# Performance work log

Measured on AMD Instinct MI355X. Metric: run time of the kernel, lower is better.

The kernel has to match this reference:

```python
import jax, jax.numpy as jnp
import numpy as np

B, N, M, F_DIM, H, D = 4, 2048, 2048, 512, 8, 64  # M == num_time
MID = H * D
EPS = 1e-5


def _layernorm(x, w, b):
    mu = jnp.mean(x, axis=-1, keepdims=True)
    var = jnp.var(x, axis=-1, keepdims=True)
    return (x - mu) * jax.lax.rsqrt(var + EPS) * w + b


def setup_inputs() -> dict:
    key = jax.random.key(0)
    ks = jax.random.split(key, 12)
    s = 0.02
    return {
        "x": jax.random.normal(ks[0], (B, N, F_DIM), jnp.float32),
        "context": jax.random.normal(ks[1], (B, M, F_DIM), jnp.float32),
        "pos_emb": jax.random.normal(ks[2], (M, F_DIM), jnp.float32) * s,  # nn.Embedding(num_time, features)
        "ln_w": jnp.ones((F_DIM,), jnp.float32),
        "ln_b": jnp.zeros((F_DIM,), jnp.float32),
        "lnc_w": jnp.ones((F_DIM,), jnp.float32),
        "lnc_b": jnp.zeros((F_DIM,), jnp.float32),
        "Wq": jax.random.normal(ks[3], (F_DIM, MID), jnp.float32) * s,
        "Wk": jax.random.normal(ks[4], (F_DIM, MID), jnp.float32) * s,
        "Wv": jax.random.normal(ks[5], (F_DIM, MID), jnp.float32) * s,
        "Wout": jax.random.normal(ks[6], (MID, F_DIM), jnp.float32) * s,
        "bout": jnp.zeros((F_DIM,), jnp.float32),
    }


def reference(x, context, pos_emb, ln_w, ln_b, lnc_w, lnc_b, Wq, Wk, Wv, Wout, bout):
    scale = D ** (-0.5)
    keys = jnp.broadcast_to(pos_emb[None], (x.shape[0], M, F_DIM))  # [B, T, F]
    xn = _layernorm(x, ln_w, ln_b)
    kn = _layernorm(keys, ln_w, ln_b)          # same norm as x (self.norm)
    cn = _layernorm(context, lnc_w, lnc_b)
    q = (xn @ Wq).reshape(x.shape[0], N, H, D).transpose(0, 2, 1, 3)  # b h n d
    k = (kn @ Wk).reshape(x.shape[0], M, H, D).transpose(0, 2, 1, 3)  # b h m d
    v = (cn @ Wv).reshape(x.shape[0], M, H, D).transpose(0, 2, 1, 3)  # b h m d
    sim = jnp.einsum('bhnd,bhmd->bhnm', q, k) * scale
    attn = jax.nn.softmax(sim, axis=-1)
    out = jnp.einsum('bhnm,bhmd->bhnd', attn, v)
    out = out.transpose(0, 2, 1, 3).reshape(x.shape[0], N, MID)  # b n (h d)
    return out @ Wout + bout
```

## Files before the change

kernel.cpp:

```cpp
#include <hip/hip_runtime.h>
#include <stdint.h>

#define B_ 4
#define N_ 2048
#define M_ 2048
#define F_ 512
#define H_ 8
#define D_ 64

typedef __bf16 bf16x8 __attribute__((ext_vector_type(8)));
typedef float f32x4 __attribute__((ext_vector_type(4)));
typedef float f32x16 __attribute__((ext_vector_type(16)));

typedef const __attribute__((address_space(1))) uint32_t* gas_ptr;
typedef __attribute__((address_space(3))) uint32_t* las_ptr;

__device__ inline ushort f32_bf16(float f) {
    union { float f; uint32_t u; } v; v.f = f;
    uint32_t r = v.u + 0x7FFFu + ((v.u >> 16) & 1u);
    return (ushort)(r >> 16);
}

__global__ __launch_bounds__(128) void ln_kernel(
    const float* __restrict__ x, const float* __restrict__ ctx, const float* __restrict__ pos,
    const float* __restrict__ lnw, const float* __restrict__ lnb,
    const float* __restrict__ lncw, const float* __restrict__ lncb,
    ushort* __restrict__ xn, ushort* __restrict__ kn, ushort* __restrict__ cn)
{
    int r = blockIdx.x;
    const float* src; ushort* dst; const float* w; const float* bp;
    if (r < B_ * N_) {
        src = x + (size_t)r * F_; dst = xn + (size_t)r * F_; w = lnw; bp = lnb;
    } else if (r < B_ * N_ + M_) {
        int rr = r - B_ * N_;
        src = pos + (size_t)rr * F_; dst = kn + (size_t)rr * F_; w = lnw; bp = lnb;
    } else {
        int rr = r - (B_ * N_ + M_);
        src = ctx + (size_t)rr * F_; dst = cn + (size_t)rr * F_; w = lncw; bp = lncb;
    }
    int tid = threadIdx.x;
    int wave = tid >> 6, lane = tid & 63;
    float4 v = reinterpret_cast<const float4*>(src)[tid];
    float s = v.x + v.y + v.z + v.w;
    float sq = v.x * v.x + v.y * v.y + v.z * v.z + v.w * v.w;
    #pragma unroll
    for (int mask = 1; mask < 64; mask <<= 1) {
        s += __shfl_xor(s, mask, 64);
        sq += __shfl_xor(sq, mask, 64);
    }
    __shared__ float red[4];
    if (lane == 0) { red[wave * 2] = s; red[wave * 2 + 1] = sq; }
    __syncthreads();
    float S = red[0] + red[2], SQ = red[1] + red[3];
    float mean = S * (1.0f / F_);
    float var = SQ * (1.0f / F_) - mean * mean;
    float rstd = rsqrtf(var + 1e-5f);
    float4 wv = reinterpret_cast<const float4*>(w)[tid];
    float4 bv = reinterpret_cast<const float4*>(bp)[tid];
    ushort4 o;
    o.x = f32_bf16((v.x - mean) * rstd * wv.x + bv.x);
    o.y = f32_bf16((v.y - mean) * rstd * wv.y + bv.y);
    o.z = f32_bf16((v.z - mean) * rstd * wv.z + bv.z);
    o.w = f32_bf16((v.w - mean) * rstd * wv.w + bv.w);
    reinterpret_cast<ushort4*>(dst)[tid] = o;
}

__global__ __launch_bounds__(256) void wtrans_kernel(
    const float* __restrict__ Wq, const float* __restrict__ Wk,
    const float* __restrict__ Wv, const float* __restrict__ Wo,
    ushort* __restrict__ WqT, ushort* __restrict__ WkT,
    ushort* __restrict__ WvT, ushort* __restrict__ WoT)
{
    const float* W; ushort* WT;
    switch (blockIdx.z) {
        case 0: W = Wq; WT = WqT; break;
        case 1: W = Wk; WT = WkT; break;
        case 2: W = Wv; WT = WvT; break;
        default: W = Wo; WT = WoT; break;
    }
    __shared__ float tile[32][33];
    int tx = threadIdx.x, ty = threadIdx.y;
    int n0 = blockIdx.x * 32, k0 = blockIdx.y * 32;
    #pragma unroll
    for (int j = 0; j < 4; ++j)
        tile[ty + j * 8][tx] = W[(size_t)(k0 + ty + j * 8) * F_ + n0 + tx];
    __syncthreads();
    #pragma unroll
    for (int j = 0; j < 4; ++j)
        WT[(size_t)(n0 + ty + j * 8) * F_ + k0 + tx] = f32_bf16(tile[tx][ty + j * 8]);
}

__device__ __forceinline__ void gemm_body(
    const ushort* __restrict__ A, const ushort* __restrict__ BT,
    const float* __restrict__ bias, void* __restrict__ Cout,
    int mode, int bx, int by)
{
    __shared__ ushort As[128][64];
    __shared__ ushort Bs[128][64];
    int tid = threadIdx.x;
    int row0 = by * 128, col0 = bx * 128;
    int wv = tid >> 6, lane = tid & 63;
    int wm = wv >> 1, wn = wv & 1;
    f32x4 acc[4][4] = {};

    const int lrow8 = lane >> 3;
    const int chs = ((lane & 7) ^ (lrow8 & 7)) * 8;
    const ushort* agp = A + (size_t)(row0 + wv * 32 + lrow8) * F_ + chs;
    const ushort* bgp = BT + (size_t)(col0 + wv * 32 + lrow8) * F_ + chs;

    for (int k0 = 0; k0 < F_; k0 += 64) {
        #pragma unroll
        for (int j = 0; j < 4; ++j) {
            __builtin_amdgcn_global_load_lds(
                (gas_ptr)(const void*)(agp + k0 + j * 8 * F_),
                (las_ptr)(void*)&As[wv * 32 + j * 8][0], 16, 0, 0);
            __builtin_amdgcn_global_load_lds(
                (gas_ptr)(const void*)(bgp + k0 + j * 8 * F_),
                (las_ptr)(void*)&Bs[wv * 32 + j * 8][0], 16, 0, 0);
        }
        __syncthreads();
        #pragma unroll
        for (int kt = 0; kt < 2; ++kt) {
            int lrow = lane & 15;
            int ch = ((kt * 4 + (lane >> 4)) ^ (lane & 7)) * 8;
            bf16x8 af[4], bfr[4];
            #pragma unroll
            for (int mt = 0; mt < 4; ++mt)
                af[mt] = *reinterpret_cast<const bf16x8*>(&As[wm * 64 + mt * 16 + lrow][ch]);
            #pragma unroll
            for (int nt = 0; nt < 4; ++nt)
                bfr[nt] = *reinterpret_cast<const bf16x8*>(&Bs[wn * 64 + nt * 16 + lrow][ch]);
            #pragma unroll
            for (int mt = 0; mt < 4; ++mt)
                #pragma unroll
                for (int nt = 0; nt < 4; ++nt)
                    acc[mt][nt] = __builtin_amdgcn_mfma_f32_16x16x32_bf16(
                        af[mt], bfr[nt], acc[mt][nt], 0, 0, 0);
        }
        __syncthreads();
    }

    int lr4 = (lane >> 4) * 4, lc = lane & 15;
    #pragma unroll
    for (int mt = 0; mt < 4; ++mt) {
        #pragma unroll
        for (int nt = 0; nt < 4; ++nt) {
            int ccol = col0 + wn * 64 + nt * 16 + lc;
            float bv = (mode == 1) ? bias[ccol] : 0.0f;
            #pragma unroll
            for (int j = 0; j < 4; ++j) {
                int crow = row0 + wm * 64 + mt * 16 + lr4 + j;
                float val = acc[mt][nt][j] + bv;
                if (mode == 1) {
                    reinterpret_cast<float*>(Cout)[(size_t)crow * F_ + ccol] = val;
                } else if (mode == 0) {
                    reinterpret_cast<ushort*>(Cout)[(size_t)crow * F_ + ccol] = f32_bf16(val);
                } else if (mode == 2) {
                    int h = ccol >> 6, t = crow >> 7, s = (crow >> 6) & 1;
                    int ab = (crow >> 5) & 1, l31 = crow & 31;
                    int ds = (ccol >> 4) & 3, g2 = (ccol >> 3) & 1, e = ccol & 7;
                    size_t addr = (((size_t)(h * 16 + t) * 16 + s * 8 + ds * 2 + ab) * 64
                                   + g2 * 32 + l31) * 8 + e;
                    reinterpret_cast<ushort*>(Cout)[addr] = f32_bf16(val);
                } else {
                    int b2 = crow >> 11, m = crow & 2047;
                    int h = ccol >> 6, d = ccol & 63;
                    int bh = b2 * 8 + h, hh = d >> 5, l31 = d & 31;
                    int t = m >> 7, s = (m >> 6) & 1, s_ = (m >> 4) & 3;
                    int g2 = (m >> 3) & 1, i = m & 7;
                    size_t addr = (((size_t)(bh * 16 + t) * 16 + hh * 8 + s * 4 + s_) * 64
                                   + g2 * 32 + l31) * 8 + i;
                    reinterpret_cast<ushort*>(Cout)[addr] = f32_bf16(val);
                }
            }
        }
    }
}

__global__ __launch_bounds__(256) void qkv_gemm_kernel(
    const ushort* __restrict__ xn, const ushort* __restrict__ kn,
    const ushort* __restrict__ cn,
    const ushort* __restrict__ WqT, const ushort* __restrict__ WkT,
    const ushort* __restrict__ WvT,
    ushort* __restrict__ qb, ushort* __restrict__ kF, ushort* __restrict__ vF)
{
    int bid = blockIdx.x;
    if (bid < 256) {
        gemm_body(xn, WqT, nullptr, (void*)qb, 0, bid & 3, bid >> 2);
    } else if (bid < 320) {
        int t = bid - 256;
        gemm_body(kn, WkT, nullptr, (void*)kF, 2, t & 3, t >> 2);
    } else {
        int t = bid - 320;
        gemm_body(cn, WvT, nullptr, (void*)vF, 3, t & 3, t >> 2);
    }
}

__global__ __launch_bounds__(256) void out_gemm_kernel(
    const ushort* __restrict__ A, const ushort* __restrict__ WoT,
    const float* __restrict__ bias, float* __restrict__ out)
{
    gemm_body(A, WoT, bias, (void*)out, 1, blockIdx.x & 3, blockIdx.x >> 2);
}

#define MAKE_PA(dst, p, ss) do {                                               \
    uint32_t w0_, w1_, w2_, w3_;                                               \
    asm("v_cvt_pk_bf16_f32 %0, %1, %2" : "=v"(w0_) : "v"(p[8*(ss)+0]), "v"(p[8*(ss)+1])); \
    asm("v_cvt_pk_bf16_f32 %0, %1, %2" : "=v"(w1_) : "v"(p[8*(ss)+2]), "v"(p[8*(ss)+3])); \
    asm("v_cvt_pk_bf16_f32 %0, %1, %2" : "=v"(w2_) : "v"(p[8*(ss)+4]), "v"(p[8*(ss)+5])); \
    asm("v_cvt_pk_bf16_f32 %0, %1, %2" : "=v"(w3_) : "v"(p[8*(ss)+6]), "v"(p[8*(ss)+7])); \
    asm("v_permlane32_swap_b32 %0, %1" : "+v"(w0_), "+v"(w2_));                \
    asm("v_permlane32_swap_b32 %0, %1" : "+v"(w1_), "+v"(w3_));                \
    union { uint32_t w[4]; bf16x8 v; } u_;                                     \
    u_.w[0] = w0_; u_.w[1] = w1_; u_.w[2] = w2_; u_.w[3] = w3_;                \
    dst = u_.v;                                                                \
} while (0)

#define KLOAD(DST, u) do {                                                     \
    const ushort* _p = kfb_ + (size_t)(u) * 4096 + lane * 8;                   \
    _Pragma("unroll")                                                          \
    for (int f_ = 0; f_ < 8; ++f_)                                             \
        DST[f_] = *reinterpret_cast<const bf16x8*>(_p + f_ * 512);             \
} while (0)

#define VLOAD(DST, u) do {                                                     \
    const ushort* _p = vfb_ + (size_t)((u) >> 1) * 8192 +                      \
                       ((u) & 1) * 4 * 512 + lane * 8;                         \
    _Pragma("unroll")                                                          \
    for (int hh_ = 0; hh_ < 2; ++hh_)                                          \
        _Pragma("unroll")                                                      \
        for (int s2_ = 0; s2_ < 4; ++s2_)                                      \
            DST[hh_ * 4 + s2_] = *reinterpret_cast<const bf16x8*>(             \
                _p + (hh_ * 8 + s2_) * 512);                                   \
} while (0)

#define COMPUTE_ONE(QF, OACC, LR) do {                                         \
    f32x16 sA, sB;                                                             \
    _Pragma("unroll")                                                          \
    for (int j = 0; j < 16; ++j) { sA[j] = 0.0f; sB[j] = 0.0f; }               \
    __builtin_amdgcn_s_setprio(1);                                             \
    _Pragma("unroll")                                                          \
    for (int ds_ = 0; ds_ < 4; ++ds_) {                                        \
        sA = __builtin_amdgcn_mfma_f32_32x32x16_bf16(kR[ds_ * 2], QF[ds_], sA, 0, 0, 0); \
        sB = __builtin_amdgcn_mfma_f32_32x32x16_bf16(kR[ds_ * 2 + 1], QF[ds_], sB, 0, 0, 0); \
    }                                                                          \
    __builtin_amdgcn_s_setprio(0);                                             \
    float p0f[16], p1f[16];                                                    \
    _Pragma("unroll")                                                          \
    for (int j = 0; j < 16; ++j)                                               \
        p0f[j] = __builtin_amdgcn_exp2f(sA[j] * c1);                           \
    _Pragma("unroll")                                                          \
    for (int j = 0; j < 16; ++j)                                               \
        p1f[j] = __builtin_amdgcn_exp2f(sB[j] * c1);                           \
    float r0 = 0.0f, r1 = 0.0f, r2 = 0.0f, r3 = 0.0f;                          \
    _Pragma("unroll")                                                          \
    for (int j = 0; j < 16; j += 4) {                                          \
        r0 += p0f[j];     r1 += p0f[j + 1];                                    \
        r2 += p0f[j + 2]; r3 += p0f[j + 3];                                    \
    }                                                                          \
    _Pragma("unroll")                                                          \
    for (int j = 0; j < 16; j += 4) {                                          \
        r0 += p1f[j];     r1 += p1f[j + 1];                                    \
        r2 += p1f[j + 2]; r3 += p1f[j + 3];                                    \
    }                                                                          \
    LR += (r0 + r1) + (r2 + r3);                                               \
    bf16x8 pa[4];                                                              \
    MAKE_PA(pa[0], p0f, 0);                                                    \
    MAKE_PA(pa[1], p0f, 1);                                                    \
    MAKE_PA(pa[2], p1f, 0);                                                    \
    MAKE_PA(pa[3], p1f, 1);                                                    \
    __builtin_amdgcn_s_setprio(1);                                             \
    _Pragma("unroll")                                                          \
    for (int hh = 0; hh < 2; ++hh)                                             \
        _Pragma("unroll")                                                      \
        for (int s_ = 0; s_ < 4; ++s_)                                         \
            OACC[hh] = __builtin_amdgcn_mfma_f32_32x32x16_bf16(                \
                pa[s_], vR[hh * 4 + s_], OACC[hh], 0, 0, 0);                   \
    __builtin_amdgcn_s_setprio(0);                                             \
} while (0)

__global__ __launch_bounds__(512, 1) void attn_kernel(
    const ushort* __restrict__ q,
    const ushort* __restrict__ kF,
    const ushort* __restrict__ vF,
    ushort* __restrict__ o)
{
    const int wave = threadIdx.x >> 6, lane = threadIdx.x & 63;
    const int l31 = lane & 31, g = lane >> 5;
    const int qpair = wave & 3, half = wave >> 2;
    const int bid = blockIdx.x;
    const int qx = bid >> 5, bh = bid & 31;
    const int b = bh >> 3, h = bh & 7;
    const int q0 = qx * 256 + qpair * 64;

    __shared__ float ols[4][64][64];
    __shared__ float lls[4][2][64];

    bf16x8 qfA[4], qfB[4];
    const ushort* qrowA = q + (size_t)(b * N_ + q0 + l31) * F_ + h * 64 + g * 8;
    const ushort* qrowB = qrowA + 32 * F_;
    #pragma unroll
    for (int ds = 0; ds < 4; ++ds) {
        qfA[ds] = *reinterpret_cast<const bf16x8*>(qrowA + ds * 16);
        qfB[ds] = *reinterpret_cast<const bf16x8*>(qrowB + ds * 16);
    }

    float l0 = 0.0f, l1 = 0.0f;
    f32x16 oaccA[2], oaccB[2];
    #pragma unroll
    for (int hh = 0; hh < 2; ++hh)
        #pragma unroll
        for (int j = 0; j < 16; ++j) { oaccA[hh][j] = 0.0f; oaccB[hh][j] = 0.0f; }

    const ushort* kfb_ = kF + (size_t)h * 16 * 16 * 512;
    const ushort* vfb_ = vF + (size_t)bh * 16 * 16 * 512;
    const float c1 = 0.18033688f;

    bf16x8 kR[8], vR[8];
    const int ubase = half * 16;

    #pragma unroll 1
    for (int uu = 0; uu < 16; ++uu) {
        int u = ubase + uu;
        KLOAD(kR, u);
        VLOAD(vR, u);
        COMPUTE_ONE(qfA, oaccA, l0);
        COMPUTE_ONE(qfB, oaccB, l1);
    }

    l0 += __shfl_xor(l0, 32, 64);
    l1 += __shfl_xor(l1, 32, 64);

    if (half) {
        #pragma unroll
        for (int hh = 0; hh < 2; ++hh)
            #pragma unroll
            for (int j = 0; j < 16; ++j) {
                ols[qpair][hh * 16 + j][lane] = oaccA[hh][j];
                ols[qpair][32 + hh * 16 + j][lane] = oaccB[hh][j];
            }
        lls[qpair][0][lane] = l0;
        lls[qpair][1][lane] = l1;
    }
    __syncthreads();
    if (!half) {
        #pragma unroll
        for (int hh = 0; hh < 2; ++hh)
            #pragma unroll
            for (int j = 0; j < 16; ++j) {
                oaccA[hh][j] += ols[qpair][hh * 16 + j][lane];
                oaccB[hh][j] += ols[qpair][32 + hh * 16 + j][lane];
            }
        l0 += lls[qpair][0][lane];
        l1 += lls[qpair][1][lane];
        float li0 = 1.0f / l0, li1 = 1.0f / l1;
        float rli0[16], rli1[16];
        #pragma unroll
        for (int j = 0; j < 16; ++j) {
            int idx = 8 * (j >> 2) + 4 * g + (j & 3);
            rli0[j] = __shfl(li0, idx, 64);
            rli1[j] = __shfl(li1, idx, 64);
        }
        #pragma unroll
        for (int hh = 0; hh < 2; ++hh)
            #pragma unroll
            for (int j = 0; j < 16; ++j) {
                int qr = (j & 3) + 8 * (j >> 2) + 4 * g;
                o[(size_t)(b * N_ + q0 + qr) * F_ + h * 64 + hh * 32 + l31] =
                    f32_bf16(oaccA[hh][j] * rli0[j]);
                o[(size_t)(b * N_ + q0 + 32 + qr) * F_ + h * 64 + hh * 32 + l31] =
                    f32_bf16(oaccB[hh][j] * rli1[j]);
            }
    }
}

extern "C" void kernel_launch(void* const* d_in, const int* in_sizes, int n_in,
                              void* d_out, int out_size, void* d_ws, size_t ws_size,
                              hipStream_t stream) {
    const float* x    = (const float*)d_in[0];
    const float* ctx  = (const float*)d_in[1];
    const float* pos  = (const float*)d_in[2];
    const float* lnw  = (const float*)d_in[3];
    const float* lnb  = (const float*)d_in[4];
    const float* lncw = (const float*)d_in[5];
    const float* lncb = (const float*)d_in[6];
    const float* Wq   = (const float*)d_in[7];
    const float* Wk   = (const float*)d_in[8];
    const float* Wv   = (const float*)d_in[9];
    const float* Wo   = (const float*)d_in[10];
    const float* bout = (const float*)d_in[11];
    float* out = (float*)d_out;

    char* ws = (char*)d_ws;
    ushort* xn  = (ushort*)(ws + 0);
    ushort* cn  = (ushort*)(ws + 8388608);
    ushort* kn  = (ushort*)(ws + 16777216);
    ushort* WqT = (ushort*)(ws + 18874368);
    ushort* WkT = (ushort*)(ws + 19398656);
    ushort* WvT = (ushort*)(ws + 19922944);
    ushort* WoT = (ushort*)(ws + 20447232);
    ushort* qb  = (ushort*)(ws + 20971520);
    ushort* kFb = (ushort*)(ws + 29360128);
    ushort* vFb = (ushort*)(ws + 39845888);
    ushort* ao  = (ushort*)(ws + 48234496);

    hipLaunchKernelGGL(ln_kernel, dim3(B_ * N_ + M_ + B_ * M_), dim3(128), 0, stream,
                       x, ctx, pos, lnw, lnb, lncw, lncb, xn, kn, cn);
    hipLaunchKernelGGL(wtrans_kernel, dim3(16, 16, 4), dim3(32, 8), 0, stream,
                       Wq, Wk, Wv, Wo, WqT, WkT, WvT, WoT);
    hipLaunchKernelGGL(qkv_gemm_kernel, dim3(576), dim3(256), 0, stream,
                       xn, kn, cn, WqT, WkT, WvT, qb, kFb, vFb);
    hipLaunchKernelGGL(attn_kernel, dim3(256), dim3(512), 0, stream,
                       qb, kFb, vFb, ao);
    hipLaunchKernelGGL(out_gemm_kernel, dim3(256), dim3(256), 0, stream,
                       ao, WoT, bout, out);
}
```

Before: 101.5 us.

## Merge layernorm and weight transpose kernels; split attention compute into halves

Combines the layernorm and weight-transpose launches into a single prep kernel whose grid covers both jobs, removing one kernel launch and its inter-kernel gap. The attention inner loop is also split so each call handles one 32-key half (one S tile, exp, P pack, PV), interleaving the two query groups. This lowers live register pressure for the S/P arrays and may give the scheduler more overlap between MFMA and exp work, at the cost of more, smaller dependency chains.

```diff
diff --git a/kernel.cpp b/kernel.cpp
--- a/kernel.cpp
+++ b/kernel.cpp
@@ -21,73 +21,76 @@
     return (ushort)(r >> 16);
 }
 
-__global__ __launch_bounds__(128) void ln_kernel(
+__global__ __launch_bounds__(128) void prep_kernel(
     const float* __restrict__ x, const float* __restrict__ ctx, const float* __restrict__ pos,
     const float* __restrict__ lnw, const float* __restrict__ lnb,
     const float* __restrict__ lncw, const float* __restrict__ lncb,
-    ushort* __restrict__ xn, ushort* __restrict__ kn, ushort* __restrict__ cn)
-{
-    int r = blockIdx.x;
-    const float* src; ushort* dst; const float* w; const float* bp;
-    if (r < B_ * N_) {
-        src = x + (size_t)r * F_; dst = xn + (size_t)r * F_; w = lnw; bp = lnb;
-    } else if (r < B_ * N_ + M_) {
-        int rr = r - B_ * N_;
-        src = pos + (size_t)rr * F_; dst = kn + (size_t)rr * F_; w = lnw; bp = lnb;
-    } else {
-        int rr = r - (B_ * N_ + M_);
-        src = ctx + (size_t)rr * F_; dst = cn + (size_t)rr * F_; w = lncw; bp = lncb;
-    }
-    int tid = threadIdx.x;
-    int wave = tid >> 6, lane = tid & 63;
-    float4 v = reinterpret_cast<const float4*>(src)[tid];
-    float s = v.x + v.y + v.z + v.w;
-    float sq = v.x * v.x + v.y * v.y + v.z * v.z + v.w * v.w;
-    #pragma unroll
-    for (int mask = 1; mask < 64; mask <<= 1) {
-        s += __shfl_xor(s, mask, 64);
-        sq += __shfl_xor(sq, mask, 64);
-    }
-    __shared__ float red[4];
-    if (lane == 0) { red[wave * 2] = s; red[wave * 2 + 1] = sq; }
-    __syncthreads();
-    float S = red[0] + red[2], SQ = red[1] + red[3];
-    float mean = S * (1.0f / F_);
-    float var = SQ * (1.0f / F_) - mean * mean;
-    float rstd = rsqrtf(var + 1e-5f);
-    float4 wv = reinterpret_cast<const float4*>(w)[tid];
-    float4 bv = reinterpret_cast<const float4*>(bp)[tid];
-    ushort4 o;
-    o.x = f32_bf16((v.x - mean) * rstd * wv.x + bv.x);
-    o.y = f32_bf16((v.y - mean) * rstd * wv.y + bv.y);
-    o.z = f32_bf16((v.z - mean) * rstd * wv.z + bv.z);
-    o.w = f32_bf16((v.w - mean) * rstd * wv.w + bv.w);
-    reinterpret_cast<ushort4*>(dst)[tid] = o;
-}
-
-__global__ __launch_bounds__(256) void wtrans_kernel(
     const float* __restrict__ Wq, const float* __restrict__ Wk,
     const float* __restrict__ Wv, const float* __restrict__ Wo,
+    ushort* __restrict__ xn, ushort* __restrict__ kn, ushort* __restrict__ cn,
     ushort* __restrict__ WqT, ushort* __restrict__ WkT,
     ushort* __restrict__ WvT, ushort* __restrict__ WoT)
 {
+    __shared__ float red[4];
+    __shared__ float tile[32][33];
+    int r = blockIdx.x;
+    int tid = threadIdx.x;
+
+    if (r < B_ * N_ + M_ + B_ * M_) {
+        const float* src; ushort* dst; const float* w; const float* bp;
+        if (r < B_ * N_) {
+            src = x + (size_t)r * F_; dst = xn + (size_t)r * F_; w = lnw; bp = lnb;
+        } else if (r < B_ * N_ + M_) {
+            int rr = r - B_ * N_;
+            src = pos + (size_t)rr * F_; dst = kn + (size_t)rr * F_; w = lnw; bp = lnb;
+        } else {
+            int rr = r - (B_ * N_ + M_);
+            src = ctx + (size_t)rr * F_; dst = cn + (size_t)rr * F_; w = lncw; bp = lncb;
+        }
+        int wave = tid >> 6, lane = tid & 63;
+        float4 v = reinterpret_cast<const float4*>(src)[tid];
+        float s = v.x + v.y + v.z + v.w;
+        float sq = v.x * v.x + v.y * v.y + v.z * v.z + v.w * v.w;
+        #pragma unroll
+        for (int mask = 1; mask < 64; mask <<= 1) {
+            s += __shfl_xor(s, mask, 64);
+            sq += __shfl_xor(sq, mask, 64);
+        }
+        if (lane == 0) { red[wave * 2] = s; red[wave * 2 + 1] = sq; }
+        __syncthreads();
+        float S = red[0] + red[2], SQ = red[1] + red[3];
+        float mean = S * (1.0f / F_);
+        float var = SQ * (1.0f / F_) - mean * mean;
+        float rstd = rsqrtf(var + 1e-5f);
+        float4 wv = reinterpret_cast<const float4*>(w)[tid];
+        float4 bv = reinterpret_cast<const float4*>(bp)[tid];
+        ushort4 o;
+        o.x = f32_bf16((v.x - mean) * rstd * wv.x + bv.x);
+        o.y = f32_bf16((v.y - mean) * rstd * wv.y + bv.y);
+        o.z = f32_bf16((v.z - mean) * rstd * wv.z + bv.z);
+        o.w = f32_bf16((v.w - mean) * rstd * wv.w + bv.w);
+        reinterpret_cast<ushort4*>(dst)[tid] = o;
+        return;
+    }
+
+    int wblk = r - (B_ * N_ + M_ + B_ * M_);
     const float* W; ushort* WT;
-    switch (blockIdx.z) {
+    switch (wblk >> 8) {
         case 0: W = Wq; WT = WqT; break;
         case 1: W = Wk; WT = WkT; break;
         case 2: W = Wv; WT = WvT; break;
         default: W = Wo; WT = WoT; break;
     }
-    __shared__ float tile[32][33];
-    int tx = threadIdx.x, ty = threadIdx.y;
-    int n0 = blockIdx.x * 32, k0 = blockIdx.y * 32;
+    int ti = wblk & 255;
+    int n0 = (ti & 15) * 32, k0 = (ti >> 4) * 32;
+    int tx = tid & 31, ty = tid >> 5;
     #pragma unroll
-    for (int j = 0; j < 4; ++j)
-        tile[ty + j * 8][tx] = W[(size_t)(k0 + ty + j * 8) * F_ + n0 + tx];
+    for (int j = 0; j < 8; ++j)
+        tile[ty + j * 4][tx] = W[(size_t)(k0 + ty + j * 4) * F_ + n0 + tx];
     __syncthreads();
     #pragma unroll
-    for (int j = 0; j < 4; ++j)
-        WT[(size_t)(n0 + ty + j * 8) * F_ + k0 + tx] = f32_bf16(tile[tx][ty + j * 8]);
+    for (int j = 0; j < 8; ++j)
+        WT[(size_t)(n0 + ty + j * 4) * F_ + k0 + tx] = f32_bf16(tile[tx][ty + j * 4]);
 }
 
 __device__ __forceinline__ void gemm_body(
@@ -234,48 +237,37 @@
                 _p + (hh_ * 8 + s2_) * 512);                                   \
 } while (0)
 
-#define COMPUTE_ONE(QF, OACC, LR) do {                                         \
-    f32x16 sA, sB;                                                             \
-    _Pragma("unroll")                                                          \
-    for (int j = 0; j < 16; ++j) { sA[j] = 0.0f; sB[j] = 0.0f; }               \
+#define COMPUTE_HALF(QF, OACC, LR, AB) do {                                    \
+    f32x16 sS;                                                                 \
+    _Pragma("unroll")                                                          \
+    for (int j = 0; j < 16; ++j) sS[j] = 0.0f;                                 \
     __builtin_amdgcn_s_setprio(1);                                             \
     _Pragma("unroll")                                                          \
-    for (int ds_ = 0; ds_ < 4; ++ds_) {                                        \
-        sA = __builtin_amdgcn_mfma_f32_32x32x16_bf16(kR[ds_ * 2], QF[ds_], sA, 0, 0, 0); \
-        sB = __builtin_amdgcn_mfma_f32_32x32x16_bf16(kR[ds_ * 2 + 1], QF[ds_], sB, 0, 0, 0); \
-    }                                                                          \
+    for (int ds_ = 0; ds_ < 4; ++ds_)                                          \
+        sS = __builtin_amdgcn_mfma_f32_32x32x16_bf16(kR[ds_ * 2 + (AB)], QF[ds_], sS, 0, 0, 0); \
     __builtin_amdgcn_s_setprio(0);                                             \
-    float p0f[16], p1f[16];                                                    \
+    float pf[16];                                                              \
     _Pragma("unroll")                                                          \
     for (int j = 0; j < 16; ++j)                                               \
-        p0f[j] = __builtin_amdgcn_exp2f(sA[j] * c1);                           \
-    _Pragma("unroll")                                                          \
-    for (int j = 0; j < 16; ++j)                                               \
-        p1f[j] = __builtin_amdgcn_exp2f(sB[j] * c1);                           \
+        pf[j] = __builtin_amdgcn_exp2f(sS[j] * c1);                            \
     float r0 = 0.0f, r1 = 0.0f, r2 = 0.0f, r3 = 0.0f;                          \
     _Pragma("unroll")                                                          \
     for (int j = 0; j < 16; j += 4) {                                          \
-        r0 += p0f[j];     r1 += p0f[j + 1];                                    \
-        r2 += p0f[j + 2]; r3 += p0f[j + 3];                                    \
-    }                                                                          \
-    _Pragma("unroll")                                                          \
-    for (int j = 0; j < 16; j += 4) {                                          \
-        r0 += p1f[j];     r1 += p1f[j + 1];                                    \
-        r2 += p1f[j + 2]; r3 += p1f[j + 3];                                    \
+        r0 += pf[j];     r1 += pf[j + 1];                                      \
+        r2 += pf[j + 2]; r3 += pf[j + 3];                                      \
     }                                                                          \
     LR += (r0 + r1) + (r2 + r3);                                               \
-    bf16x8 pa[4];                                                              \
-    MAKE_PA(pa[0], p0f, 0);                                                    \
-    MAKE_PA(pa[1], p0f, 1);                                                    \
-    MAKE_PA(pa[2], p1f, 0);                                                    \
-    MAKE_PA(pa[3], p1f, 1);                                                    \
+    bf16x8 pa0, pa1;                                                           \
+    MAKE_PA(pa0, pf, 0);                                                       \
+    MAKE_PA(pa1, pf, 1);                                                       \
     __builtin_amdgcn_s_setprio(1);                                             \
     _Pragma("unroll")                                                          \
-    for (int hh = 0; hh < 2; ++hh)                                             \
-        _Pragma("unroll")                                                      \
-        for (int s_ = 0; s_ < 4; ++s_)                                         \
-            OACC[hh] = __builtin_amdgcn_mfma_f32_32x32x16_bf16(                \
-                pa[s_], vR[hh * 4 + s_], OACC[hh], 0, 0, 0);                   \
+    for (int hh = 0; hh < 2; ++hh) {                                           \
+        OACC[hh] = __builtin_amdgcn_mfma_f32_32x32x16_bf16(                    \
+            pa0, vR[hh * 4 + (AB) * 2], OACC[hh], 0, 0, 0);                    \
+        OACC[hh] = __builtin_amdgcn_mfma_f32_32x32x16_bf16(                    \
+            pa1, vR[hh * 4 + (AB) * 2 + 1], OACC[hh], 0, 0, 0);                \
+    }                                                                          \
     __builtin_amdgcn_s_setprio(0);                                             \
 } while (0)
 
@@ -324,8 +316,10 @@
         int u = ubase + uu;
         KLOAD(kR, u);
         VLOAD(vR, u);
-        COMPUTE_ONE(qfA, oaccA, l0);
-        COMPUTE_ONE(qfB, oaccB, l1);
+        COMPUTE_HALF(qfA, oaccA, l0, 0);
+        COMPUTE_HALF(qfB, oaccB, l1, 0);
+        COMPUTE_HALF(qfA, oaccA, l0, 1);
+        COMPUTE_HALF(qfB, oaccB, l1, 1);
     }
 
     l0 += __shfl_xor(l0, 32, 64);
@@ -404,10 +398,10 @@
     ushort* vFb = (ushort*)(ws + 39845888);
     ushort* ao  = (ushort*)(ws + 48234496);
 
-    hipLaunchKernelGGL(ln_kernel, dim3(B_ * N_ + M_ + B_ * M_), dim3(128), 0, stream,
-                       x, ctx, pos, lnw, lnb, lncw, lncb, xn, kn, cn);
-    hipLaunchKernelGGL(wtrans_kernel, dim3(16, 16, 4), dim3(32, 8), 0, stream,
-                       Wq, Wk, Wv, Wo, WqT, WkT, WvT, WoT);
+    hipLaunchKernelGGL(prep_kernel, dim3(B_ * N_ + M_ + B_ * M_ + 1024), dim3(128),
+                       0, stream,
+                       x, ctx, pos, lnw, lnb, lncw, lncb, Wq, Wk, Wv, Wo,
+                       xn, kn, cn, WqT, WkT, WvT, WoT);
     hipLaunchKernelGGL(qkv_gemm_kernel, dim3(576), dim3(256), 0, stream,
                        xn, kn, cn, WqT, WkT, WvT, qb, kFb, vFb);
     hipLaunchKernelGGL(attn_kernel, dim3(256), dim3(512), 0, stream,
```

Result: faster. 92.47 us, median of 2 (-8.9%).
